# Kernel tuning notes

Hardware: AMD Instinct MI355X
Metric: run time of the kernel (lower is better)

Reference implementation:

```python
import jax, jax.numpy as jnp
import numpy as np

B, I, H = 16384, 1024, 1024
LN_EPS = 1e-5


def setup_inputs() -> dict:
    key = jax.random.key(0)
    k1, k2, k3, k4 = jax.random.split(key, 4)
    x = jax.random.normal(k1, (B, I), dtype=jnp.float32)
    h_out = jax.random.normal(k2, (B, H), dtype=jnp.float32)
    cell = jax.random.normal(k3, (B, H), dtype=jnp.float32)
    # nn.Linear(i_size + h, 4*h, bias=False): weight shape [4h, i+h]
    W = jax.random.normal(k4, (4 * H, I + H), dtype=jnp.float32) * (1.0 / np.sqrt(I + H))
    gamma = jnp.ones((4, H), dtype=jnp.float32)
    beta = jnp.zeros((4, H), dtype=jnp.float32)
    return {"x": x, "h_out": h_out, "cell": cell, "W": W, "gamma": gamma, "beta": beta}


def reference(x, h_out, cell, W, gamma, beta):
    # concat + linear -> [B, 4, H]
    cat = jnp.concatenate([x, h_out], axis=-1)               # [B, I+H]
    t = (cat @ W.T).reshape(cat.shape[0], 4, H)              # [B, 4, H]
    # LayerNorm over normalized_shape=(4, H): stats over last two dims
    mu = jnp.mean(t, axis=(-2, -1), keepdims=True)
    var = jnp.mean(jnp.square(t - mu), axis=(-2, -1), keepdims=True)
    handle = (t - mu) * jax.lax.rsqrt(var + LN_EPS) * gamma + beta
    # gates: first 3 slices sigmoid, last slice GELU (exact, eval-mode dropout = identity)
    gates = jax.nn.sigmoid(handle[:, 0:3, :])
    f_gate, i_gate, o_gate = gates[:, 0], gates[:, 1], gates[:, 2]
    h_cand = jax.nn.gelu(handle[:, 3, :], approximate=False)
    new_cell = f_gate * cell + i_gate * h_cand
    new_out = o_gate * new_cell
    return (new_out, new_cell)
```

## Files before the change

### kernel.cpp

```cpp
#include <hip/hip_runtime.h>
#include <stdint.h>

#define B_ROWS 16384
#define IN_DIM 1024
#define H_DIM  1024
#define KDIM   2048
#define NDIM   4096
#define LN_EPSF 1e-5f

typedef unsigned short u16;
typedef float  f32x4  __attribute__((ext_vector_type(4)));
typedef float  fv4    __attribute__((ext_vector_type(4)));
typedef __bf16 bf16x8 __attribute__((ext_vector_type(8)));
typedef u16    u16x4  __attribute__((ext_vector_type(4)));
typedef u16    u16x8  __attribute__((ext_vector_type(8)));

__device__ __forceinline__ u16 f2bf(float f) {
  unsigned u = __float_as_uint(f);
  u += 0x7FFFu + ((u >> 16) & 1u);
  return (u16)(u >> 16);
}
__device__ __forceinline__ float bf2f(u16 s) {
  return __uint_as_float(((unsigned)s) << 16);
}

#define GLOAD_LDS16(gp, lp) __builtin_amdgcn_global_load_lds( \
    (__attribute__((address_space(1))) void*)(gp),            \
    (__attribute__((address_space(3))) void*)(lp), 16, 0, 0)

__global__ __launch_bounds__(256) void cast_concat(
    const float* __restrict__ x, const float* __restrict__ h,
    u16* __restrict__ cat) {
  int idx = blockIdx.x * 256 + threadIdx.x;
  long base = (long)idx * 8;
  int  c = (int)(base & (KDIM - 1));
  long b = base >> 11;
  const float* src = (c < IN_DIM) ? (x + b * IN_DIM + c)
                                  : (h + b * H_DIM + (c - IN_DIM));
  fv4 v0 = *(const fv4*)(src);
  fv4 v1 = *(const fv4*)(src + 4);
  u16x8 o;
  o[0]=f2bf(v0[0]); o[1]=f2bf(v0[1]); o[2]=f2bf(v0[2]); o[3]=f2bf(v0[3]);
  o[4]=f2bf(v1[0]); o[5]=f2bf(v1[1]); o[6]=f2bf(v1[2]); o[7]=f2bf(v1[3]);
  *(u16x8*)(cat + base) = o;
}

__global__ __launch_bounds__(256) void cast_plain(
    const float* __restrict__ w, u16* __restrict__ wb) {
  int idx = blockIdx.x * 256 + threadIdx.x;
  long base = (long)idx * 8;
  fv4 v0 = *(const fv4*)(w + base);
  fv4 v1 = *(const fv4*)(w + base + 4);
  u16x8 o;
  o[0]=f2bf(v0[0]); o[1]=f2bf(v0[1]); o[2]=f2bf(v0[2]); o[3]=f2bf(v0[3]);
  o[4]=f2bf(v1[0]); o[5]=f2bf(v1[1]); o[6]=f2bf(v1[2]); o[7]=f2bf(v1[3]);
  *(u16x8*)(wb + base) = o;
}


#define STA(S_, P_, T_) GLOAD_LDS16(pA + (size_t)(P_) * 64 * KDIM + (T_) * 64, \
                                    &LA[S_][(P_) * 4096 + tid * 8])
#define STB(S_, P_, T_) GLOAD_LDS16(pB + (size_t)(P_) * 64 * KDIM + (T_) * 64, \
                                    &LB[S_][(P_) * 4096 + tid * 8])

#define RDAB(S_) {                                                            \
    const u16* ap_ = &LA[S_][abase];                                          \
    const u16* bp_ = &LB[S_][bbase];                                          \
    a[0][0]  = *(const bf16x8*)(ap_ + 0 * 1024 + kk0);                        \
    a[1][0]  = *(const bf16x8*)(ap_ + 1 * 1024 + kk0);                        \
    a[2][0]  = *(const bf16x8*)(ap_ + 2 * 1024 + kk0);                        \
    a[3][0]  = *(const bf16x8*)(ap_ + 3 * 1024 + kk0);                        \
    b0[0][0] = *(const bf16x8*)(bp_ + 0 * 1024 + kk0);                        \
    b0[1][0] = *(const bf16x8*)(bp_ + 1 * 1024 + kk0);                        \
    a[0][1]  = *(const bf16x8*)(ap_ + 0 * 1024 + kk1);                        \
    a[1][1]  = *(const bf16x8*)(ap_ + 1 * 1024 + kk1);                        \
    a[2][1]  = *(const bf16x8*)(ap_ + 2 * 1024 + kk1);                        \
    a[3][1]  = *(const bf16x8*)(ap_ + 3 * 1024 + kk1);                        \
    b0[0][1] = *(const bf16x8*)(bp_ + 0 * 1024 + kk1);                        \
    b0[1][1] = *(const bf16x8*)(bp_ + 1 * 1024 + kk1); }

#define RDA4(S_) {                                                            \
    const u16* ap_ = &LA[S_][abase + 4096];                                   \
    a[0][0] = *(const bf16x8*)(ap_ + 0 * 1024 + kk0);                         \
    a[1][0] = *(const bf16x8*)(ap_ + 1 * 1024 + kk0);                         \
    a[2][0] = *(const bf16x8*)(ap_ + 2 * 1024 + kk0);                         \
    a[3][0] = *(const bf16x8*)(ap_ + 3 * 1024 + kk0);                         \
    a[0][1] = *(const bf16x8*)(ap_ + 0 * 1024 + kk1);                         \
    a[1][1] = *(const bf16x8*)(ap_ + 1 * 1024 + kk1);                         \
    a[2][1] = *(const bf16x8*)(ap_ + 2 * 1024 + kk1);                         \
    a[3][1] = *(const bf16x8*)(ap_ + 3 * 1024 + kk1); }

#define RDB2(S_) {                                                            \
    const u16* bp_ = &LB[S_][bbase + 2048];                                   \
    b1[0][0] = *(const bf16x8*)(bp_ + 0 * 1024 + kk0);                        \
    b1[1][0] = *(const bf16x8*)(bp_ + 1 * 1024 + kk0);                        \
    b1[0][1] = *(const bf16x8*)(bp_ + 0 * 1024 + kk1);                        \
    b1[1][1] = *(const bf16x8*)(bp_ + 1 * 1024 + kk1); }

#define MQK(MB_, NB_, V_, KS_)                                                \
  _Pragma("unroll") for (int m_ = 0; m_ < 4; ++m_)                            \
  _Pragma("unroll") for (int n_ = 0; n_ < 2; ++n_)                            \
    acc[(MB_) + m_][(NB_) + n_] = __builtin_amdgcn_mfma_f32_16x16x32_bf16(    \
        a[m_][KS_], V_[n_][KS_], acc[(MB_) + m_][(NB_) + n_], 0, 0, 0);

#define PH_ENTER(N_)                                                          \
  __builtin_amdgcn_sched_barrier(0);                                          \
  __builtin_amdgcn_s_barrier();                                               \
  asm volatile("s_waitcnt lgkmcnt(" #N_ ")" ::: "memory");                    \
  __builtin_amdgcn_sched_barrier(0);                                          \
  __builtin_amdgcn_s_setprio(1);

#define PH_MID                                                                \
  asm volatile("s_waitcnt lgkmcnt(0)" ::: "memory");                          \
  __builtin_amdgcn_sched_barrier(0);

#define PH_EXIT                                                               \
  __builtin_amdgcn_s_setprio(0);                                              \
  __builtin_amdgcn_sched_barrier(0);                                          \
  __builtin_amdgcn_s_barrier();

#define ITER(U_, ST_) do {                                                    \
                                                                      \
    RDAB(0);                                                                  \
    STA(1, 1, (U_) + 1); STA(1, 3, (U_) + 1);                                 \
    PH_ENTER(6); MQK(0, 0, b0, 0); PH_MID; MQK(0, 0, b0, 1); PH_EXIT;         \
                                                                      \
    RDB2(0);                                                                  \
    if (ST_) { STA(0, 0, (U_) + 2); STA(0, 2, (U_) + 2); }                    \
    PH_ENTER(2); MQK(0, 2, b1, 0); PH_MID; MQK(0, 2, b1, 1); PH_EXIT;         \
                                                                      \
    RDA4(0);                                                                  \
    if (ST_) { STB(0, 0, (U_) + 2); STB(0, 1, (U_) + 2); }                    \
    PH_ENTER(4); MQK(4, 0, b0, 0); PH_MID; MQK(4, 0, b0, 1); PH_EXIT;         \
                                  \
    if (ST_) { STB(0, 2, (U_) + 2); STB(0, 3, (U_) + 2); }                    \
    PH_ENTER(0); MQK(4, 2, b1, 0); MQK(4, 2, b1, 1);                          \
    __builtin_amdgcn_s_setprio(0);                                            \
    __builtin_amdgcn_sched_barrier(0);                                        \
    if (ST_) { asm volatile("s_waitcnt vmcnt(4)" ::: "memory"); }             \
    else     { asm volatile("s_waitcnt vmcnt(0)" ::: "memory"); }             \
    __builtin_amdgcn_s_barrier();                                             \
                                                                      \
    RDAB(1);                                                                  \
    if (ST_) { STA(0, 1, (U_) + 2); STA(0, 3, (U_) + 2); }                    \
    PH_ENTER(6); MQK(0, 0, b0, 0); PH_MID; MQK(0, 0, b0, 1); PH_EXIT;         \
                                                                      \
    RDB2(1);                                                                  \
    if (ST_) { STA(1, 0, (U_) + 3); STA(1, 2, (U_) + 3); }                    \
    PH_ENTER(2); MQK(0, 2, b1, 0); PH_MID; MQK(0, 2, b1, 1); PH_EXIT;         \
                                                                      \
    RDA4(1);                                                                  \
    if (ST_) { STB(1, 0, (U_) + 3); STB(1, 1, (U_) + 3); }                    \
    PH_ENTER(4); MQK(4, 0, b0, 0); PH_MID; MQK(4, 0, b0, 1); PH_EXIT;         \
                                 \
    if (ST_) { STB(1, 2, (U_) + 3); STB(1, 3, (U_) + 3); }                    \
    PH_ENTER(0); MQK(4, 2, b1, 0); MQK(4, 2, b1, 1);                          \
    __builtin_amdgcn_s_setprio(0);                                            \
    __builtin_amdgcn_sched_barrier(0);                                        \
    if (ST_) { asm volatile("s_waitcnt vmcnt(6)" ::: "memory"); }             \
    __builtin_amdgcn_s_barrier();                                             \
  } while (0)

__global__ __launch_bounds__(512, 2) void gemm_bt(
    const u16* __restrict__ A,
    const u16* __restrict__ Bw,
    u16* __restrict__ C) {
  __shared__ u16 LA[2][16384];
  __shared__ u16 LB[2][16384];

  const int tid  = threadIdx.x;
  const int lane = tid & 63;
  const int wave = tid >> 6;
  const int wm   = wave >> 2;
  const int wn   = wave & 3;
  const int r    = lane & 15;
  const int g    = lane >> 4;

  const int bid = blockIdx.x;
  const int xcd = bid & 7;
  const int k_  = bid >> 3;
  const int row0 = (xcd * 8 + (k_ >> 4)) * 256;
  const int col0 = (k_ & 15) * 256;

  const int l    = tid ^ ((tid >> 3) & 7);
  const int srow = l >> 3;
  const int skc  = (l & 7) * 8;
  const u16* pA = A  + (size_t)(row0 + srow) * KDIM + skc;
  const u16* pB = Bw + (size_t)(col0 + srow) * KDIM + skc;

  const int rx   = r & 7;
  const int kk0  = ((g      ) ^ rx) << 3;
  const int kk1  = (((4 | g)) ^ rx) << 3;
  const int abase = wm * 8192 + r * 64;
  const int bbase = wn * 4096 + r * 64;

  f32x4 acc[8][4] = {};
  bf16x8 a[4][2], b0[2][2], b1[2][2];

  STA(0, 0, 0); STA(0, 1, 0); STA(0, 2, 0); STA(0, 3, 0);
  STB(0, 0, 0); STB(0, 1, 0); STB(0, 2, 0); STB(0, 3, 0);
  STA(1, 0, 1); STA(1, 2, 1);
  STB(1, 0, 1); STB(1, 1, 1); STB(1, 2, 1); STB(1, 3, 1);
  asm volatile("s_waitcnt vmcnt(6)" ::: "memory");
  __builtin_amdgcn_s_barrier();

  for (int it = 0; it < 15; ++it) {
    ITER(2 * it, 1);
  }
  ITER(30, 0);

#pragma unroll
  for (int m = 0; m < 8; ++m)
#pragma unroll
    for (int n = 0; n < 4; ++n)
#pragma unroll
      for (int q = 0; q < 4; ++q) {
        const int rr = row0 + wm * 128 + m * 16 + g * 4 + q;
        const int cc = col0 + wn * 64 + n * 16 + r;
        C[(size_t)rr * NDIM + cc] = f2bf(acc[m][n][q]);
      }
}

__global__ __launch_bounds__(256) void ln_gates(
    const u16* __restrict__ t,
    const float* __restrict__ cell,
    const float* __restrict__ gamma,
    const float* __restrict__ beta,
    float* __restrict__ out) {
  const int b   = blockIdx.x;
  const int tid = threadIdx.x;
  const int h0  = tid * 4;

  const u16* trow = t + (long)b * NDIM;
  float v[4][4];
#pragma unroll
  for (int gi = 0; gi < 4; ++gi) {
    u16x4 raw = *(const u16x4*)&trow[gi * H_DIM + h0];
#pragma unroll
    for (int j = 0; j < 4; ++j) v[gi][j] = bf2f(raw[j]);
  }

  float s1 = 0.f, s2 = 0.f;
#pragma unroll
  for (int gi = 0; gi < 4; ++gi)
#pragma unroll
    for (int j = 0; j < 4; ++j) { s1 += v[gi][j]; s2 += v[gi][j] * v[gi][j]; }

#pragma unroll
  for (int m = 32; m; m >>= 1) {
    s1 += __shfl_xor(s1, m);
    s2 += __shfl_xor(s2, m);
  }
  __shared__ float red[2][4];
  const int wave = tid >> 6, lane = tid & 63;
  if (lane == 0) { red[0][wave] = s1; red[1][wave] = s2; }
  __syncthreads();
  s1 = red[0][0] + red[0][1] + red[0][2] + red[0][3];
  s2 = red[1][0] + red[1][1] + red[1][2] + red[1][3];

  const float mean  = s1 * (1.f / (float)NDIM);
  const float var   = s2 * (1.f / (float)NDIM) - mean * mean;
  const float scale = rsqrtf(var + LN_EPSF);

  float hd[4][4];
#pragma unroll
  for (int gi = 0; gi < 4; ++gi) {
    fv4 gm = *(const fv4*)&gamma[gi * H_DIM + h0];
    fv4 bt = *(const fv4*)&beta[gi * H_DIM + h0];
#pragma unroll
    for (int j = 0; j < 4; ++j)
      hd[gi][j] = (v[gi][j] - mean) * scale * gm[j] + bt[j];
  }

  fv4 cv = *(const fv4*)&cell[(long)b * H_DIM + h0];
  fv4 no, nc;
#pragma unroll
  for (int j = 0; j < 4; ++j) {
    float fg = 1.f / (1.f + expf(-hd[0][j]));
    float ig = 1.f / (1.f + expf(-hd[1][j]));
    float og = 1.f / (1.f + expf(-hd[2][j]));
    float hc = 0.5f * hd[3][j] * (1.f + erff(hd[3][j] * 0.70710678118654752f));
    float ncell = fg * cv[j] + ig * hc;
    nc[j] = ncell;
    no[j] = og * ncell;
  }
  *(fv4*)&out[(long)b * H_DIM + h0] = no;
  *(fv4*)&out[(long)B_ROWS * H_DIM + (long)b * H_DIM + h0] = nc;
}

extern "C" void kernel_launch(void* const* d_in, const int* in_sizes, int n_in,
                              void* d_out, int out_size, void* d_ws, size_t ws_size,
                              hipStream_t stream) {
  const float* x     = (const float*)d_in[0];
  const float* h     = (const float*)d_in[1];
  const float* cell  = (const float*)d_in[2];
  const float* W     = (const float*)d_in[3];
  const float* gamma = (const float*)d_in[4];
  const float* beta  = (const float*)d_in[5];
  float* out = (float*)d_out;

  const size_t cat_bytes = (size_t)B_ROWS * KDIM * sizeof(u16);
  const size_t w_bytes   = (size_t)NDIM * KDIM * sizeof(u16);
  const size_t t_bytes   = (size_t)B_ROWS * NDIM * sizeof(u16);
  if (ws_size < cat_bytes + w_bytes + t_bytes) return;

  uint8_t* ws = (uint8_t*)d_ws;
  u16* catb = (u16*)ws;
  u16* Wb   = (u16*)(ws + cat_bytes);
  u16* tbuf = (u16*)(ws + cat_bytes + w_bytes);

  cast_concat<<<(B_ROWS * (long)KDIM / 8) / 256, 256, 0, stream>>>(x, h, catb);
  cast_plain<<<(NDIM * (long)KDIM / 8) / 256, 256, 0, stream>>>(W, Wb);

  gemm_bt<<<dim3(1024), 512, 0, stream>>>(catb, Wb, tbuf);

  ln_gates<<<B_ROWS, 256, 0, stream>>>(tbuf, cell, gamma, beta, out);
}
```

Measured before the change: 365.3 us.

## Prefetch B fragments one phase earlier in the GEMM main loop

Moves the LDS reads of B fragments earlier: the second B half is loaded together with the first A half, and the next tile's first B half is read during the previous phase. The prologue is reordered so B tile 1 arrives before the A halves and an initial B read happens before the loop. Waitcnt thresholds are adjusted so each phase waits only for the fragments it needs, which is meant to hide more LDS latency behind MFMAs. It adds register pressure, and the vmcnt bookkeeping is fragile, so an ordering mistake could read stale LDS.

New measurement: 382.0 us. 4.6% more time.

```diff
diff --git a/kernel.cpp b/kernel.cpp
--- a/kernel.cpp
+++ b/kernel.cpp
@@ -63,24 +63,7 @@
 #define STB(S_, P_, T_) GLOAD_LDS16(pB + (size_t)(P_) * 64 * KDIM + (T_) * 64, \
                                     &LB[S_][(P_) * 4096 + tid * 8])
 
-#define RDAB(S_) {                                                            \
-    const u16* ap_ = &LA[S_][abase];                                          \
-    const u16* bp_ = &LB[S_][bbase];                                          \
-    a[0][0]  = *(const bf16x8*)(ap_ + 0 * 1024 + kk0);                        \
-    a[1][0]  = *(const bf16x8*)(ap_ + 1 * 1024 + kk0);                        \
-    a[2][0]  = *(const bf16x8*)(ap_ + 2 * 1024 + kk0);                        \
-    a[3][0]  = *(const bf16x8*)(ap_ + 3 * 1024 + kk0);                        \
-    b0[0][0] = *(const bf16x8*)(bp_ + 0 * 1024 + kk0);                        \
-    b0[1][0] = *(const bf16x8*)(bp_ + 1 * 1024 + kk0);                        \
-    a[0][1]  = *(const bf16x8*)(ap_ + 0 * 1024 + kk1);                        \
-    a[1][1]  = *(const bf16x8*)(ap_ + 1 * 1024 + kk1);                        \
-    a[2][1]  = *(const bf16x8*)(ap_ + 2 * 1024 + kk1);                        \
-    a[3][1]  = *(const bf16x8*)(ap_ + 3 * 1024 + kk1);                        \
-    b0[0][1] = *(const bf16x8*)(bp_ + 0 * 1024 + kk1);                        \
-    b0[1][1] = *(const bf16x8*)(bp_ + 1 * 1024 + kk1); }
-
-#define RDA4(S_) {                                                            \
-    const u16* ap_ = &LA[S_][abase + 4096];                                   \
+#define RDA_(S_, OFF_) { const u16* ap_ = &LA[S_][abase + (OFF_)];            \
     a[0][0] = *(const bf16x8*)(ap_ + 0 * 1024 + kk0);                         \
     a[1][0] = *(const bf16x8*)(ap_ + 1 * 1024 + kk0);                         \
     a[2][0] = *(const bf16x8*)(ap_ + 2 * 1024 + kk0);                         \
@@ -90,12 +73,11 @@
     a[2][1] = *(const bf16x8*)(ap_ + 2 * 1024 + kk1);                         \
     a[3][1] = *(const bf16x8*)(ap_ + 3 * 1024 + kk1); }
 
-#define RDB2(S_) {                                                            \
-    const u16* bp_ = &LB[S_][bbase + 2048];                                   \
-    b1[0][0] = *(const bf16x8*)(bp_ + 0 * 1024 + kk0);                        \
-    b1[1][0] = *(const bf16x8*)(bp_ + 1 * 1024 + kk0);                        \
-    b1[0][1] = *(const bf16x8*)(bp_ + 0 * 1024 + kk1);                        \
-    b1[1][1] = *(const bf16x8*)(bp_ + 1 * 1024 + kk1); }
+#define RDB_(S_, V_, NB_) { const u16* bp_ = &LB[S_][bbase + (NB_) * 1024];   \
+    V_[0][0] = *(const bf16x8*)(bp_ + 0 * 1024 + kk0);                        \
+    V_[1][0] = *(const bf16x8*)(bp_ + 1 * 1024 + kk0);                        \
+    V_[0][1] = *(const bf16x8*)(bp_ + 0 * 1024 + kk1);                        \
+    V_[1][1] = *(const bf16x8*)(bp_ + 1 * 1024 + kk1); }
 
 #define MQK(MB_, NB_, V_, KS_)                                                \
   _Pragma("unroll") for (int m_ = 0; m_ < 4; ++m_)                            \
@@ -103,61 +85,63 @@
     acc[(MB_) + m_][(NB_) + n_] = __builtin_amdgcn_mfma_f32_16x16x32_bf16(    \
         a[m_][KS_], V_[n_][KS_], acc[(MB_) + m_][(NB_) + n_], 0, 0, 0);
 
-#define PH_ENTER(N_)                                                          \
+#define ENTER(N_)                                                             \
   __builtin_amdgcn_sched_barrier(0);                                          \
   __builtin_amdgcn_s_barrier();                                               \
   asm volatile("s_waitcnt lgkmcnt(" #N_ ")" ::: "memory");                    \
   __builtin_amdgcn_sched_barrier(0);                                          \
   __builtin_amdgcn_s_setprio(1);
 
-#define PH_MID                                                                \
-  asm volatile("s_waitcnt lgkmcnt(0)" ::: "memory");                          \
+#define MID(N_)                                                               \
+  asm volatile("s_waitcnt lgkmcnt(" #N_ ")" ::: "memory");                    \
   __builtin_amdgcn_sched_barrier(0);
 
-#define PH_EXIT                                                               \
+#define EXITP                                                                 \
   __builtin_amdgcn_s_setprio(0);                                              \
   __builtin_amdgcn_sched_barrier(0);                                          \
   __builtin_amdgcn_s_barrier();
 
+#define EXITV(N_)                                                             \
+  __builtin_amdgcn_s_setprio(0);                                              \
+  __builtin_amdgcn_sched_barrier(0);                                          \
+  asm volatile("s_waitcnt vmcnt(" #N_ ")" ::: "memory");                      \
+  __builtin_amdgcn_s_barrier();
+
 #define ITER(U_, ST_) do {                                                    \
-                                                                      \
-    RDAB(0);                                                                  \
+                     \
+    RDA_(0, 0); RDB_(0, b1, 2);                                               \
     STA(1, 1, (U_) + 1); STA(1, 3, (U_) + 1);                                 \
-    PH_ENTER(6); MQK(0, 0, b0, 0); PH_MID; MQK(0, 0, b0, 1); PH_EXIT;         \
-                                                                      \
-    RDB2(0);                                                                  \
+    ENTER(8); MQK(0, 0, b0, 0); MID(4); MQK(0, 0, b0, 1); EXITP;              \
+                                     \
     if (ST_) { STA(0, 0, (U_) + 2); STA(0, 2, (U_) + 2); }                    \
-    PH_ENTER(2); MQK(0, 2, b1, 0); PH_MID; MQK(0, 2, b1, 1); PH_EXIT;         \
-                                                                      \
-    RDA4(0);                                                                  \
+    ENTER(0); MQK(0, 2, b1, 0); MQK(0, 2, b1, 1); EXITP;                      \
+                    \
+    RDA_(0, 4096);                                                            \
     if (ST_) { STB(0, 0, (U_) + 2); STB(0, 1, (U_) + 2); }                    \
-    PH_ENTER(4); MQK(4, 0, b0, 0); PH_MID; MQK(4, 0, b0, 1); PH_EXIT;         \
-                                  \
+    ENTER(4); MQK(4, 0, b0, 0); MID(0); MQK(4, 0, b0, 1); EXITV(6);           \
+                    \
+    RDB_(1, b0, 0);                                                           \
     if (ST_) { STB(0, 2, (U_) + 2); STB(0, 3, (U_) + 2); }                    \
-    PH_ENTER(0); MQK(4, 2, b1, 0); MQK(4, 2, b1, 1);                          \
-    __builtin_amdgcn_s_setprio(0);                                            \
-    __builtin_amdgcn_sched_barrier(0);                                        \
-    if (ST_) { asm volatile("s_waitcnt vmcnt(4)" ::: "memory"); }             \
-    else     { asm volatile("s_waitcnt vmcnt(0)" ::: "memory"); }             \
-    __builtin_amdgcn_s_barrier();                                             \
-                                                                      \
-    RDAB(1);                                                                  \
+    ENTER(4); MQK(4, 2, b1, 0); MQK(4, 2, b1, 1); EXITV(4);                   \
+                                     \
+    RDA_(1, 0); RDB_(1, b1, 2);                                               \
     if (ST_) { STA(0, 1, (U_) + 2); STA(0, 3, (U_) + 2); }                    \
-    PH_ENTER(6); MQK(0, 0, b0, 0); PH_MID; MQK(0, 0, b0, 1); PH_EXIT;         \
-                                                                      \
-    RDB2(1);                                                                  \
+    ENTER(8); MQK(0, 0, b0, 0); MID(4); MQK(0, 0, b0, 1); EXITP;              \
+                                                            \
     if (ST_) { STA(1, 0, (U_) + 3); STA(1, 2, (U_) + 3); }                    \
-    PH_ENTER(2); MQK(0, 2, b1, 0); PH_MID; MQK(0, 2, b1, 1); PH_EXIT;         \
-                                                                      \
-    RDA4(1);                                                                  \
+    ENTER(0); MQK(0, 2, b1, 0); MQK(0, 2, b1, 1); EXITP;                      \
+                             \
+    RDA_(1, 4096);                                                            \
     if (ST_) { STB(1, 0, (U_) + 3); STB(1, 1, (U_) + 3); }                    \
-    PH_ENTER(4); MQK(4, 0, b0, 0); PH_MID; MQK(4, 0, b0, 1); PH_EXIT;         \
-                                 \
+    ENTER(4); MQK(4, 0, b0, 0); MID(0); MQK(4, 0, b0, 1); EXITV(6);           \
+                                       \
+    if (ST_) { RDB_(0, b0, 0); }                                              \
     if (ST_) { STB(1, 2, (U_) + 3); STB(1, 3, (U_) + 3); }                    \
-    PH_ENTER(0); MQK(4, 2, b1, 0); MQK(4, 2, b1, 1);                          \
+    ENTER(4); MQK(4, 2, b1, 0); MQK(4, 2, b1, 1);                             \
     __builtin_amdgcn_s_setprio(0);                                            \
     __builtin_amdgcn_sched_barrier(0);                                        \
     if (ST_) { asm volatile("s_waitcnt vmcnt(6)" ::: "memory"); }             \
+    else     { asm volatile("s_waitcnt vmcnt(0)" ::: "memory"); }             \
     __builtin_amdgcn_s_barrier();                                             \
   } while (0)
 
@@ -199,10 +183,11 @@
 
   STA(0, 0, 0); STA(0, 1, 0); STA(0, 2, 0); STA(0, 3, 0);
   STB(0, 0, 0); STB(0, 1, 0); STB(0, 2, 0); STB(0, 3, 0);
+  STB(1, 0, 1); STB(1, 1, 1); STB(1, 2, 1); STB(1, 3, 1);
   STA(1, 0, 1); STA(1, 2, 1);
-  STB(1, 0, 1); STB(1, 1, 1); STB(1, 2, 1); STB(1, 3, 1);
   asm volatile("s_waitcnt vmcnt(6)" ::: "memory");
   __builtin_amdgcn_s_barrier();
+  RDB_(0, b0, 0);
 
   for (int it = 0; it < 15; ++it) {
     ITER(2 * it, 1);
```
